# Optimization experiments

Measured on AMD Instinct MI355X. Metric: run time of the kernel, lower is better.

## Reference

```python
import jax, jax.numpy as jnp
import numpy as np

LN_EPS = 1e-5  # torch nn.LayerNorm default

def _layer_norm(x, w, b):
    m = jnp.mean(x, axis=-1, keepdims=True)
    v = jnp.mean(jnp.square(x - m), axis=-1, keepdims=True)
    return (x - m) * jax.lax.rsqrt(v + LN_EPS) * w + b

def setup_inputs() -> dict:
    R, N, D, A = 8, 8192, 2048, 128
    init_scale = 0.01
    key = jax.random.key(0)
    k0, k1, k2 = jax.random.split(key, 3)
    x = jax.random.normal(k0, (N, D), jnp.float32)
    ln_w = jnp.ones((R, D), jnp.float32)              # per-router input LayerNorm weight
    ln_b = jnp.zeros((R, D), jnp.float32)
    router_weights = jax.random.normal(k1, (R, D, A), jnp.float32) * init_scale
    rw_ln_w = jax.random.normal(k2, (R, D), jnp.float32) * init_scale  # weight-LN gamma (init ones*scale in src)
    rw_ln_b = jnp.zeros((R, D), jnp.float32)
    router_bias = jnp.zeros((R, A), jnp.float32)
    return {"x": x, "ln_w": ln_w, "ln_b": ln_b, "router_weights": router_weights,
            "rw_ln_w": rw_ln_w, "rw_ln_b": rw_ln_b, "router_bias": router_bias}

def reference(x, ln_w, ln_b, router_weights, rw_ln_w, rw_ln_b, router_bias):
    # Per-router LayerNorm of shared input x: new_x [R, N, D]
    new_x = jax.vmap(lambda w, b: _layer_norm(x, w, b))(ln_w, ln_b)
    # normalize_router_weights=True: LayerNorm over in_dim of W[i].T, then transpose back
    rw_norm = jax.vmap(lambda W, w, b: _layer_norm(W.T, w, b).T)(router_weights, rw_ln_w, rw_ln_b)  # [R, D, A]
    adapter_logits = jnp.einsum('rnd,rda->rna', new_x, rw_norm) + router_bias[:, None, :]
    adapter_probs = jax.nn.softmax(adapter_logits, axis=-1)
    return new_x, adapter_logits, adapter_probs
```

## Files before the change

### kernel.cpp

```cpp
#include <hip/hip_runtime.h>
#include <hip/hip_bf16.h>
#include <stdint.h>

#define R_ 8
#define N_ 8192
#define D_ 2048
#define A_ 128
#define J_ 1024
#define LN_EPS 1e-5f

typedef __attribute__((ext_vector_type(8))) short bf16x8;
typedef __attribute__((ext_vector_type(4))) float f32x4;

__device__ inline ushort f2bf(float f) {
    union { float f; uint32_t u; } v; v.f = f;
    uint32_t u = v.u;
    return (ushort)((u + 0x7fffu + ((u >> 16) & 1u)) >> 16);
}
__device__ inline float bf2f(ushort u) {
    union { uint32_t u; float f; } v; v.u = ((uint32_t)u) << 16;
    return v.f;
}

__global__ __launch_bounds__(256) void k_lnx(
    const float* __restrict__ x,
    const float* __restrict__ W,
    const float* __restrict__ ln_w,
    const float* __restrict__ ln_b,
    const float* __restrict__ rw_w,
    const float* __restrict__ rw_b,
    const float* __restrict__ rbias,
    ushort* __restrict__ xhat,
    ushort* __restrict__ Bt,
    float* __restrict__ cvec,
    float* __restrict__ new_x)
{
    __shared__ float sm[16];
    const int t = threadIdx.x;
    const int g = blockIdx.x / 9;
    const int i = blockIdx.x % 9;

    if (i < 8) {
        const int n = g * 8 + i;
        const float* xr = x + (size_t)n * D_;
        float4 v0 = *(const float4*)(xr + t * 4);
        float4 v1 = *(const float4*)(xr + 1024 + t * 4);
        float s  = v0.x + v0.y + v0.z + v0.w + v1.x + v1.y + v1.z + v1.w;
        float sq = v0.x*v0.x + v0.y*v0.y + v0.z*v0.z + v0.w*v0.w
                 + v1.x*v1.x + v1.y*v1.y + v1.z*v1.z + v1.w*v1.w;
        #pragma unroll
        for (int o = 32; o > 0; o >>= 1) {
            s  += __shfl_xor(s,  o, 64);
            sq += __shfl_xor(sq, o, 64);
        }
        if ((t & 63) == 0) { sm[t >> 6] = s; sm[8 + (t >> 6)] = sq; }
        __syncthreads();
        s  = sm[0] + sm[1] + sm[2] + sm[3];
        sq = sm[8] + sm[9] + sm[10] + sm[11];
        const float mean = s * (1.0f / D_);
        const float var  = sq * (1.0f / D_) - mean * mean;
        const float rstd = rsqrtf(var + LN_EPS);

        float4 h0, h1;
        h0.x = (v0.x - mean) * rstd; h0.y = (v0.y - mean) * rstd;
        h0.z = (v0.z - mean) * rstd; h0.w = (v0.w - mean) * rstd;
        h1.x = (v1.x - mean) * rstd; h1.y = (v1.y - mean) * rstd;
        h1.z = (v1.z - mean) * rstd; h1.w = (v1.w - mean) * rstd;

        ushort4 p0 = make_ushort4(f2bf(h0.x), f2bf(h0.y), f2bf(h0.z), f2bf(h0.w));
        ushort4 p1 = make_ushort4(f2bf(h1.x), f2bf(h1.y), f2bf(h1.z), f2bf(h1.w));
        *(ushort4*)(xhat + (size_t)n * D_ + t * 4)        = p0;
        *(ushort4*)(xhat + (size_t)n * D_ + 1024 + t * 4) = p1;

        #pragma unroll
        for (int r = 0; r < R_; ++r) {
            const float* wr = ln_w + (size_t)r * D_;
            const float* br = ln_b + (size_t)r * D_;
            const float4 w0 = *(const float4*)(wr + t * 4);
            const float4 b0 = *(const float4*)(br + t * 4);
            const float4 w1 = *(const float4*)(wr + 1024 + t * 4);
            const float4 b1 = *(const float4*)(br + 1024 + t * 4);
            f32x4 o0, o1;
            o0[0] = h0.x * w0.x + b0.x; o0[1] = h0.y * w0.y + b0.y;
            o0[2] = h0.z * w0.z + b0.z; o0[3] = h0.w * w0.w + b0.w;
            o1[0] = h1.x * w1.x + b1.x; o1[1] = h1.y * w1.y + b1.y;
            o1[2] = h1.z * w1.z + b1.z; o1[3] = h1.w * w1.w + b1.w;
            float* dst = new_x + ((size_t)r * N_ + n) * D_;
            __builtin_nontemporal_store(o0, (f32x4*)(dst + t * 4));
            __builtin_nontemporal_store(o1, (f32x4*)(dst + 1024 + t * 4));
        }
    } else {
        const int j = g;
        const int r = j >> 7, a = j & 127;
        const float* Wc = W + (size_t)r * D_ * A_ + a;

        float vals[8];
        float s = 0.f, sq = 0.f;
        #pragma unroll
        for (int k = 0; k < 8; ++k) {
            float v = Wc[(size_t)(t + k * 256) * A_];
            vals[k] = v; s += v; sq += v * v;
        }
        #pragma unroll
        for (int o = 32; o > 0; o >>= 1) {
            s  += __shfl_xor(s,  o, 64);
            sq += __shfl_xor(sq, o, 64);
        }
        if ((t & 63) == 0) { sm[t >> 6] = s; sm[8 + (t >> 6)] = sq; }
        __syncthreads();
        s  = sm[0] + sm[1] + sm[2] + sm[3];
        sq = sm[8] + sm[9] + sm[10] + sm[11];
        const float mean = s * (1.0f / D_);
        const float var  = sq * (1.0f / D_) - mean * mean;
        const float rstd = rsqrtf(var + LN_EPS);

        float cp = 0.f;
        #pragma unroll
        for (int k = 0; k < 8; ++k) {
            const int d = t + k * 256;
            const float nv = (vals[k] - mean) * rstd * rw_w[(size_t)r * D_ + d]
                           + rw_b[(size_t)r * D_ + d];
            Bt[(size_t)j * D_ + d] = f2bf(ln_w[(size_t)r * D_ + d] * nv);
            cp += ln_b[(size_t)r * D_ + d] * nv;
        }
        __syncthreads();
        #pragma unroll
        for (int o = 32; o > 0; o >>= 1) cp += __shfl_xor(cp, o, 64);
        if ((t & 63) == 0) sm[t >> 6] = cp;
        __syncthreads();
        if (t == 0) cvec[j] = sm[0] + sm[1] + sm[2] + sm[3] + rbias[(size_t)r * A_ + a];
    }
}

__global__ __launch_bounds__(256) void k_gemm(
    const ushort* __restrict__ Xh,
    const ushort* __restrict__ Bt,
    const float* __restrict__ cvec,
    float* __restrict__ logits,
    float* __restrict__ probs)
{
    __shared__ __attribute__((aligned(16))) ushort As[64 * 64];
    __shared__ __attribute__((aligned(16))) ushort Bs[128 * 64];

    const int t    = threadIdx.x;
    const int lane = t & 63;
    const int w    = t >> 6;
    const int r    = blockIdx.x & 7;
    const int mt   = blockIdx.x >> 3;
    const int m0   = mt * 64;
    const int j0   = r * 128;

    f32x4 acc[8];
    #pragma unroll
    for (int jf = 0; jf < 8; ++jf) acc[jf] = (f32x4){0.f, 0.f, 0.f, 0.f};

    for (int kt = 0; kt < 32; ++kt) {
        __syncthreads();
        #pragma unroll
        for (int c = 0; c < 2; ++c) {
            const int q    = t + c * 256;
            const int row  = q >> 3;
            const int slot = q & 7;
            const int kc   = slot ^ (row & 7);
            const ushort* gA = Xh + (size_t)(m0 + row) * D_ + kt * 64 + kc * 8;
            __builtin_amdgcn_global_load_lds(
                (const __attribute__((address_space(1))) void*)gA,
                (__attribute__((address_space(3))) void*)(&As[q * 8]), 16, 0, 0);
        }
        #pragma unroll
        for (int c = 0; c < 4; ++c) {
            const int q    = t + c * 256;
            const int row  = q >> 3;
            const int slot = q & 7;
            const int kc   = slot ^ (row & 7);
            const ushort* gB = Bt + (size_t)(j0 + row) * D_ + kt * 64 + kc * 8;
            __builtin_amdgcn_global_load_lds(
                (const __attribute__((address_space(1))) void*)gB,
                (__attribute__((address_space(3))) void*)(&Bs[q * 8]), 16, 0, 0);
        }
        __syncthreads();

        #pragma unroll
        for (int kf = 0; kf < 2; ++kf) {
            const int slot  = (lane >> 4) + 4 * kf;
            const int pslot = slot ^ (lane & 7);
            const bf16x8 afr = *(const bf16x8*)(&As[(w * 16 + (lane & 15)) * 64
                                                    + pslot * 8]);
            #pragma unroll
            for (int jf = 0; jf < 8; ++jf) {
                const bf16x8 bfr = *(const bf16x8*)(&Bs[(jf * 16 + (lane & 15)) * 64
                                                        + pslot * 8]);
                acc[jf] = __builtin_amdgcn_mfma_f32_16x16x32_bf16(afr, bfr, acc[jf], 0, 0, 0);
            }
        }
    }

    float cv[8];
    #pragma unroll
    for (int jf = 0; jf < 8; ++jf) cv[jf] = cvec[j0 + jf * 16 + (lane & 15)];

    #pragma unroll
    for (int reg = 0; reg < 4; ++reg) {
        const int row = m0 + w * 16 + (lane >> 4) * 4 + reg;
        float v[8], e[8];
        float mx = -3.4e38f;
        #pragma unroll
        for (int jf = 0; jf < 8; ++jf) {
            v[jf] = acc[jf][reg] + cv[jf];
            mx = fmaxf(mx, v[jf]);
        }
        #pragma unroll
        for (int o = 8; o > 0; o >>= 1) mx = fmaxf(mx, __shfl_xor(mx, o, 64));
        float ssum = 0.f;
        #pragma unroll
        for (int jf = 0; jf < 8; ++jf) { e[jf] = __expf(v[jf] - mx); ssum += e[jf]; }
        #pragma unroll
        for (int o = 8; o > 0; o >>= 1) ssum += __shfl_xor(ssum, o, 64);
        const float inv = 1.0f / ssum;
        float* lrow = logits + ((size_t)r * N_ + row) * A_;
        float* prow = probs  + ((size_t)r * N_ + row) * A_;
        #pragma unroll
        for (int jf = 0; jf < 8; ++jf) {
            const int aa = jf * 16 + (lane & 15);
            __builtin_nontemporal_store(v[jf], lrow + aa);
            __builtin_nontemporal_store(e[jf] * inv, prow + aa);
        }
    }
}

extern "C" void kernel_launch(void* const* d_in, const int* in_sizes, int n_in,
                              void* d_out, int out_size, void* d_ws, size_t ws_size,
                              hipStream_t stream)
{
    const float* x     = (const float*)d_in[0];
    const float* ln_w  = (const float*)d_in[1];
    const float* ln_b  = (const float*)d_in[2];
    const float* W     = (const float*)d_in[3];
    const float* rw_w  = (const float*)d_in[4];
    const float* rw_b  = (const float*)d_in[5];
    const float* rbias = (const float*)d_in[6];

    float* out    = (float*)d_out;
    float* new_x  = out;
    float* logits = out + (size_t)R_ * N_ * D_;
    float* probs  = logits + (size_t)R_ * N_ * A_;

    ushort* xhat = (ushort*)d_ws;
    ushort* Btp  = (ushort*)((char*)d_ws + (size_t)N_ * D_ * 2);
    float*  cvec = (float*)((char*)d_ws + (size_t)N_ * D_ * 2 + (size_t)J_ * D_ * 2);

    hipLaunchKernelGGL(k_lnx,  dim3(9 * J_), dim3(256), 0, stream,
                       x, W, ln_w, ln_b, rw_w, rw_b, rbias, xhat, Btp, cvec, new_x);
    hipLaunchKernelGGL(k_gemm, dim3(J_),     dim3(256), 0, stream,
                       xhat, Btp, cvec, logits, probs);
}
```

Baseline: 163.8 us.

## Double-buffer LDS tiles in router GEMM to overlap loads with MFMA

The GEMM kernel now keeps two LDS buffers for the A and B tiles and issues the async global-to-LDS loads for the next K tile before computing on the current one. Partial vmcnt waits and explicit barriers replace the two full syncthreads per iteration, so memory latency can overlap with MFMA work. This doubles LDS use per block (48KB), which may lower occupancy, and it depends on the vmcnt(6) count matching the number of outstanding loads per stage.

```diff
diff --git a/kernel.cpp b/kernel.cpp
--- a/kernel.cpp
+++ b/kernel.cpp
@@ -139,8 +139,8 @@
     float* __restrict__ logits,
     float* __restrict__ probs)
 {
-    __shared__ __attribute__((aligned(16))) ushort As[64 * 64];
-    __shared__ __attribute__((aligned(16))) ushort Bs[128 * 64];
+    __shared__ __attribute__((aligned(16))) ushort As[2][64 * 64];
+    __shared__ __attribute__((aligned(16))) ushort Bs[2][128 * 64];
 
     const int t    = threadIdx.x;
     const int lane = t & 63;
@@ -150,12 +150,7 @@
     const int m0   = mt * 64;
     const int j0   = r * 128;
 
-    f32x4 acc[8];
-    #pragma unroll
-    for (int jf = 0; jf < 8; ++jf) acc[jf] = (f32x4){0.f, 0.f, 0.f, 0.f};
-
-    for (int kt = 0; kt < 32; ++kt) {
-        __syncthreads();
+    auto stage = [&](int buf, int kt) {
         #pragma unroll
         for (int c = 0; c < 2; ++c) {
             const int q    = t + c * 256;
@@ -165,7 +160,7 @@
             const ushort* gA = Xh + (size_t)(m0 + row) * D_ + kt * 64 + kc * 8;
             __builtin_amdgcn_global_load_lds(
                 (const __attribute__((address_space(1))) void*)gA,
-                (__attribute__((address_space(3))) void*)(&As[q * 8]), 16, 0, 0);
+                (__attribute__((address_space(3))) void*)(&As[buf][q * 8]), 16, 0, 0);
         }
         #pragma unroll
         for (int c = 0; c < 4; ++c) {
@@ -176,24 +171,47 @@
             const ushort* gB = Bt + (size_t)(j0 + row) * D_ + kt * 64 + kc * 8;
             __builtin_amdgcn_global_load_lds(
                 (const __attribute__((address_space(1))) void*)gB,
-                (__attribute__((address_space(3))) void*)(&Bs[q * 8]), 16, 0, 0);
-        }
-        __syncthreads();
-
+                (__attribute__((address_space(3))) void*)(&Bs[buf][q * 8]), 16, 0, 0);
+        }
+    };
+
+    f32x4 acc[8];
+    #pragma unroll
+    for (int jf = 0; jf < 8; ++jf) acc[jf] = (f32x4){0.f, 0.f, 0.f, 0.f};
+
+    auto mfma_tile = [&](int buf) {
         #pragma unroll
         for (int kf = 0; kf < 2; ++kf) {
             const int slot  = (lane >> 4) + 4 * kf;
             const int pslot = slot ^ (lane & 7);
-            const bf16x8 afr = *(const bf16x8*)(&As[(w * 16 + (lane & 15)) * 64
-                                                    + pslot * 8]);
+            const bf16x8 afr = *(const bf16x8*)(&As[buf][(w * 16 + (lane & 15)) * 64
+                                                         + pslot * 8]);
             #pragma unroll
             for (int jf = 0; jf < 8; ++jf) {
-                const bf16x8 bfr = *(const bf16x8*)(&Bs[(jf * 16 + (lane & 15)) * 64
-                                                        + pslot * 8]);
+                const bf16x8 bfr = *(const bf16x8*)(&Bs[buf][(jf * 16 + (lane & 15)) * 64
+                                                             + pslot * 8]);
                 acc[jf] = __builtin_amdgcn_mfma_f32_16x16x32_bf16(afr, bfr, acc[jf], 0, 0, 0);
             }
         }
+    };
+
+    stage(0, 0);
+    for (int kt = 0; kt < 31; ++kt) {
+        const int cur = kt & 1;
+        stage(cur ^ 1, kt + 1);
+        asm volatile("s_waitcnt vmcnt(6)" ::: "memory");
+        __builtin_amdgcn_sched_barrier(0);
+        __builtin_amdgcn_s_barrier();
+        __builtin_amdgcn_sched_barrier(0);
+        mfma_tile(cur);
+        __builtin_amdgcn_s_barrier();
+        __builtin_amdgcn_sched_barrier(0);
     }
+    asm volatile("s_waitcnt vmcnt(0)" ::: "memory");
+    __builtin_amdgcn_sched_barrier(0);
+    __builtin_amdgcn_s_barrier();
+    __builtin_amdgcn_sched_barrier(0);
+    mfma_tile(1);
 
     float cv[8];
     #pragma unroll
```

Measured after the change: 181.2 us. 1.11x slower.
